# Kernel optimization log

Measured on AMD Instinct MI355X. Metric: run time of the kernel, lower is better.

The kernel has to match this reference:

```python
import jax, jax.numpy as jnp
import numpy as np

NHEAD = 8
DC = 32
IN_CHS = 2 * NHEAD  # cross_coverage and self_coverage both True
EPS = 1e-5  # BatchNorm1d default eps


def conv2d(x, w, pad):
    return jax.lax.conv_general_dilated(
        x, w, window_strides=(1, 1), padding=[(pad, pad), (pad, pad)],
        dimension_numbers=('NCHW', 'OIHW', 'NCHW'))


def setup_inputs() -> dict:
    key = jax.random.key(0)
    ks = jax.random.split(key, 10)
    b, t, H, W = 8, 256, 16, 32
    l = H * W
    prev_attn = jax.random.uniform(ks[0], (b * NHEAD, t, l), dtype=jnp.float32)
    curr_attn = jax.random.uniform(ks[1], (b * NHEAD, t, l), dtype=jnp.float32)
    key_padding_mask = jax.random.uniform(ks[2], (b, l)) < 0.25  # True = padded
    conv_w = jax.random.normal(ks[3], (DC, IN_CHS, 5, 5), jnp.float32) * 0.05
    conv_b = jnp.zeros((DC,), jnp.float32)
    proj_w = jax.random.normal(ks[4], (NHEAD, DC, 1, 1), jnp.float32) * 0.05
    g_w1 = jax.random.normal(ks[5], (IN_CHS // 2, IN_CHS, 3, 3), jnp.float32) * 0.05
    g_b1 = jnp.zeros((IN_CHS // 2,), jnp.float32)
    g_w2 = jax.random.normal(ks[6], (IN_CHS, IN_CHS // 2, 1, 1), jnp.float32) * 0.05
    g_b2 = jnp.zeros((IN_CHS,), jnp.float32)
    bn_gamma = jnp.ones((NHEAD,), jnp.float32)
    bn_beta = jnp.zeros((NHEAD,), jnp.float32)
    return dict(prev_attn=prev_attn, key_padding_mask=key_padding_mask, h=H,
                curr_attn=curr_attn, tgt_vocab=113,
                conv_w=conv_w, conv_b=conv_b, proj_w=proj_w,
                g_w1=g_w1, g_b1=g_b1, g_w2=g_w2, g_b2=g_b2,
                bn_gamma=bn_gamma, bn_beta=bn_beta)


def reference(prev_attn, key_padding_mask, h, curr_attn, tgt_vocab,
              conv_w, conv_b, proj_w, g_w1, g_b1, g_w2, g_b2, bn_gamma, bn_beta):
    n = NHEAD
    b = prev_attn.shape[0] // n
    t = curr_attn.shape[1]
    l = key_padding_mask.shape[1]
    w = l // h

    prev = prev_attn.reshape(b, n, t, l)
    curr = curr_attn.reshape(b, n, t, l)
    attns = jnp.concatenate([prev, curr], axis=1)  # [b, 2n, t, l]
    c = attns.shape[1]

    # gating network on per-step attention images: [(b t), c, h, w]
    attns_bt = attns.transpose(0, 2, 1, 3).reshape(b * t, c, h, w)
    g = jax.nn.relu(conv2d(attns_bt, g_w1, 1) + g_b1[None, :, None, None])
    g = g.mean(axis=(2, 3))  # AdaptiveAvgPool2d((1,1)) -> [(b t), c//2]
    g = jax.nn.sigmoid(jnp.einsum('bi,oi->bo', g, g_w2[:, :, 0, 0]) + g_b2)
    gate = g.reshape(b, t, c).transpose(0, 2, 1)[..., None]  # [b, c, t, 1]

    gated = attns * gate
    cum = jnp.cumsum(gated, axis=2) - gated  # exclusive cumulative coverage
    cum2d = cum.transpose(0, 2, 1, 3).reshape(b * t, c, h, w)

    mask = jnp.broadcast_to(key_padding_mask.reshape(b, 1, 1, h, w),
                            (b, t, 1, h, w)).reshape(b * t, 1, h, w)

    cov = jax.nn.relu(conv2d(cum2d, conv_w, 2) + conv_b[None, :, None, None])
    cov = jnp.where(mask, 0.0, cov)
    cov = jnp.einsum('bdhw,nd->bnhw', cov, proj_w[:, :, 0, 0])  # 1x1 proj, no bias

    # MaskBatchNorm2d: BN statistics over non-masked positions only
    nm = (~mask).astype(cov.dtype)  # [(b t), 1, h, w]
    cnt = nm.sum()
    mean = (cov * nm).sum(axis=(0, 2, 3), keepdims=True) / cnt  # per-channel
    var = (jnp.square(cov - mean) * nm).sum(axis=(0, 2, 3), keepdims=True) / cnt
    xn = (cov - mean) * jax.lax.rsqrt(var + EPS) * bn_gamma[None, :, None, None] \
        + bn_beta[None, :, None, None]
    cov = jnp.where(mask, cov, xn)  # masked positions keep pre-BN values (zeros)

    out = cov.reshape(b, t, n, l).transpose(0, 2, 1, 3).reshape(b * n, t, l)
    return out
```

## Files before the change

### kernel.cpp

```cpp
#include <hip/hip_runtime.h>
#include <hip/hip_bf16.h>

#define BB   8
#define TT   256
#define NH   8
#define CC   16
#define HH   16
#define WW   32
#define LL   512
#define DCH  32
#define GC   8

#define PSC  1928
#define PSG  1736

typedef __attribute__((ext_vector_type(8))) short s8b;
typedef __attribute__((ext_vector_type(4))) float f32x4;

__device__ __forceinline__ ushort f2bfu(float v) {
  __hip_bfloat16 h = __float2bfloat16(v);
  ushort s;
  __builtin_memcpy(&s, &h, 2);
  return s;
}

__global__ __launch_bounds__(256) void k_gen(const float* __restrict__ cw,
                                             const float* __restrict__ pw,
                                             const float* __restrict__ gw1,
                                             ushort* __restrict__ bfrag,
                                             ushort* __restrict__ pwf,
                                             ushort* __restrict__ bfragG,
                                             float* __restrict__ sums) {
  int idx = blockIdx.x * 256 + threadIdx.x;
  if (idx < 17) sums[idx] = 0.f;
  if (idx < 13312) {
    int j = idx & 7, lane = (idx >> 3) & 63, nt = (idx >> 9) & 1, s = idx >> 10;
    int quad = lane >> 4, col = lane & 15;
    int k = s * 32 + quad * 8 + j;
    int n = nt * 16 + col;
    float v = (k < 400) ? cw[(n * CC + (k & 15)) * 25 + (k >> 4)] : 0.f;
    bfrag[idx] = f2bfu(v);
  } else if (idx < 13824) {
    int i2 = idx - 13312;
    int j = i2 & 7, lane = i2 >> 3;
    int quad = lane >> 4, col = lane & 15;
    float v = (col < NH) ? pw[col * DCH + quad * 8 + j] : 0.f;
    pwf[i2] = f2bfu(v);
  } else if (idx < 16384) {
    int i3 = idx - 13824;
    int j = i3 & 7, lane = (i3 >> 3) & 63, s = i3 >> 9;
    int quad = lane >> 4, col = lane & 15;
    int k = s * 32 + quad * 8 + j;
    float v = 0.f;
    if (k < 144 && col < GC) v = gw1[(col * CC + (k & 15)) * 9 + (k >> 4)];
    bfragG[i3] = f2bfu(v);
  }
}

__global__ __launch_bounds__(256) void k_gate(
    const float* __restrict__ prev, const float* __restrict__ curr,
    const ushort* __restrict__ bfragG, const float* __restrict__ gb1,
    const float* __restrict__ gw2, const float* __restrict__ gb2,
    float* __restrict__ gate2) {
  __shared__ __align__(16) ushort img[8 * PSG];
  __shared__ float redg[64];
  __shared__ float pooled[16];

  int tid = threadIdx.x;
  int lane = tid & 63, w = tid >> 6;
  int bt = blockIdx.x;
  int b = bt >> 8, t = bt & 255;
  int quad = lane >> 4, col = lane & 15;
  int qh = quad >> 1, icb = (quad & 1) * 8;

  for (int i = tid; i < PSG; i += 256) ((uint4*)img)[i] = (uint4){0, 0, 0, 0};
  __syncthreads();

#pragma unroll
  for (int it = 0; it < 4; ++it) {
#pragma unroll
    for (int e = 0; e < 2; ++e) {
      int W = ((it * 4 + w) * 2 + e) * 64 + lane;
      int cp = W >> 8, pp = W & 255;
      int l0 = pp * 2;
      const float* src = (cp < 4) ? prev : curr;
      int chb = (cp & 3) * 2;
      const float* p0 = src + ((size_t)(b * NH + chb) * TT + t) * LL + l0;
      float2 fa = *(const float2*)p0;
      float2 fb = *(const float2*)(p0 + TT * LL);
      unsigned lo = (unsigned)f2bfu(fa.x) | ((unsigned)f2bfu(fb.x) << 16);
      unsigned hi = (unsigned)f2bfu(fa.y) | ((unsigned)f2bfu(fb.y) << 16);
      int r = l0 >> 5, x = l0 & 31;
      int slot = (r + 1) * 48 + 8 + x;
      *(uint2*)&img[cp * PSG + slot * 2] = (uint2){lo, hi};
    }
  }
  __syncthreads();

  f32x4 acc[8];
#pragma unroll
  for (int mi = 0; mi < 8; ++mi) acc[mi] = (f32x4){0.f, 0.f, 0.f, 0.f};
  int mtbase = w * 8;
  int ab[8];
#pragma unroll
  for (int mi = 0; mi < 8; ++mi) {
    int mt = mtbase + mi;
    int py = mt >> 1, px = ((mt & 1) << 4) + col;
    ab[mi] = (icb >> 1) * PSG + (py * 48 + 7 + px) * 2;
  }
  const int offE[5] = {0, 2, 49, 96, 98};
  const int offO[5] = {1, 48, 50, 97, 98};
  const s8b* bG = (const s8b*)bfragG;
#pragma unroll
  for (int s = 0; s < 5; ++s) {
    s8b bf = bG[s * 64 + lane];
    int off2 = (qh ? offO[s] : offE[s]) * 2;
#pragma unroll
    for (int mi = 0; mi < 8; ++mi) {
      union { unsigned u[4]; s8b v; } A;
      int a0 = ab[mi] + off2;
#pragma unroll
      for (int p = 0; p < 4; ++p) A.u[p] = *(const unsigned*)&img[a0 + p * PSG];
      acc[mi] = __builtin_amdgcn_mfma_f32_16x16x32_bf16(A.v, bf, acc[mi], 0, 0, 0);
    }
  }

  float gb1c = (col < GC) ? gb1[col] : 0.f;
  float s = 0.f;
#pragma unroll
  for (int mi = 0; mi < 8; ++mi)
#pragma unroll
    for (int r = 0; r < 4; ++r) s += fmaxf(acc[mi][r] + gb1c, 0.f);
  s += __shfl_down(s, 16, 64);
  s += __shfl_down(s, 32, 64);
  if (lane < 16) redg[w * 16 + lane] = s;
  __syncthreads();
  if (tid < 16)
    pooled[tid] = (redg[tid] + redg[16 + tid] + redg[32 + tid] + redg[48 + tid]) *
                  (1.0f / (float)LL);
  __syncthreads();
  if (tid < 16) {
    float z = gb2[tid];
#pragma unroll
    for (int i = 0; i < GC; ++i) z = fmaf(pooled[i], gw2[tid * GC + i], z);
    gate2[(b * CC + tid) * TT + t] = 1.f / (1.f + __expf(-z));
  }
}

__global__ __launch_bounds__(256) void k_cumA(const float* __restrict__ prev,
                                              const float* __restrict__ curr,
                                              const float* __restrict__ gate2,
                                              float* __restrict__ csum) {
  int idx = blockIdx.x * 256 + threadIdx.x;
  int l = idx & 511, tc = (idx >> 9) & 7, c = (idx >> 12) & 15, b = idx >> 16;
  const float* src = (c < NH) ? prev : curr;
  const float* a = src + ((size_t)(b * NH + (c & 7)) * TT + tc * 32) * LL + l;
  const float* g = gate2 + (b * CC + c) * TT + tc * 32;
  float s = 0.f;
#pragma unroll 8
  for (int j = 0; j < 32; ++j) s = fmaf(a[(size_t)j * LL], g[j], s);
  csum[((b * CC + c) * 8 + tc) * LL + l] = s;
}

__global__ __launch_bounds__(256) void k_cumB(const float* __restrict__ prev,
                                              const float* __restrict__ curr,
                                              const float* __restrict__ gate2,
                                              const float* __restrict__ csum,
                                              ushort* __restrict__ cum) {
  int idx = blockIdx.x * 256 + threadIdx.x;
  int l = idx & 511, tc = (idx >> 9) & 7, c = (idx >> 12) & 15, b = idx >> 16;
  float run = 0.f;
  const float* cs = csum + ((b * CC + c) * 8) * LL + l;
  for (int u = 0; u < tc; ++u) run += cs[u * LL];
  const float* src = (c < NH) ? prev : curr;
  const float* a = src + ((size_t)(b * NH + (c & 7)) * TT + tc * 32) * LL + l;
  const float* g = gate2 + (b * CC + c) * TT + tc * 32;
  ushort* o = cum + ((size_t)(b * CC + c) * TT + tc * 32) * LL + l;
#pragma unroll 4
  for (int j = 0; j < 32; ++j) {
    o[(size_t)j * LL] = f2bfu(run);
    run = fmaf(a[(size_t)j * LL], g[j], run);
  }
}

__global__ __launch_bounds__(256, 2) void k_cov(
    const ushort* __restrict__ cum, const ushort* __restrict__ bfrag,
    const ushort* __restrict__ pwf, const float* __restrict__ cb,
    const int* __restrict__ mask, float* __restrict__ out,
    float* __restrict__ sums) {
  __shared__ __align__(16) ushort img[8 * PSC];
  __shared__ __align__(16) ushort scr[4 * 640];
  __shared__ float redp[128];
  __shared__ float redc[4];

  int tid = threadIdx.x;
  int lane = tid & 63, w = tid >> 6;
  int bt = blockIdx.x;
  int b = bt >> 8, t = bt & 255;
  int quad = lane >> 4, col = lane & 15;
  int qh = quad >> 1, icb = (quad & 1) * 8;

  for (int i = tid; i < PSC; i += 256) ((uint4*)img)[i] = (uint4){0, 0, 0, 0};
  __syncthreads();

#pragma unroll
  for (int it = 0; it < 4; ++it) {
#pragma unroll
    for (int e = 0; e < 2; ++e) {
      int W = ((it * 4 + w) * 2 + e) * 64 + lane;
      int cp = W >> 8, pp = W & 255;
      int l0 = pp * 2;
      const ushort* p0 = cum + ((size_t)(b * CC + cp * 2) * TT + t) * LL + l0;
      unsigned a = *(const unsigned*)p0;
      unsigned bb2 = *(const unsigned*)(p0 + TT * LL);
      unsigned lo = (a & 0xFFFFu) | (bb2 << 16);
      unsigned hi = (a >> 16) | (bb2 & 0xFFFF0000u);
      int r = l0 >> 5, x = l0 & 31;
      int slot = (r + 2) * 48 + 8 + x;
      *(uint2*)&img[cp * PSC + slot * 2] = (uint2){lo, hi};
    }
  }
  __syncthreads();

  f32x4 acc[8][2];
#pragma unroll
  for (int mi = 0; mi < 8; ++mi) {
    acc[mi][0] = (f32x4){0.f, 0.f, 0.f, 0.f};
    acc[mi][1] = (f32x4){0.f, 0.f, 0.f, 0.f};
  }
  int mtbase = w * 8;
  int ab[8];
#pragma unroll
  for (int mi = 0; mi < 8; ++mi) {
    int mt = mtbase + mi;
    int py = mt >> 1, px = ((mt & 1) << 4) + col;
    ab[mi] = (icb >> 1) * PSC + (py * 48 + 6 + px) * 2;
  }
  const int offE[13] = {0, 2, 4, 49, 51, 96, 98, 100, 145, 147, 192, 194, 196};
  const int offO[13] = {1, 3, 48, 50, 52, 97, 99, 144, 146, 148, 193, 195, 196};
  const s8b* bfr = (const s8b*)bfrag;
#pragma unroll
  for (int s = 0; s < 13; ++s) {
    s8b bf0 = bfr[(s * 2) * 64 + lane];
    s8b bf1 = bfr[(s * 2 + 1) * 64 + lane];
    int off2 = (qh ? offO[s] : offE[s]) * 2;
#pragma unroll
    for (int mi = 0; mi < 8; ++mi) {
      union { unsigned u[4]; s8b v; } A;
      int a0 = ab[mi] + off2;
#pragma unroll
      for (int p = 0; p < 4; ++p) A.u[p] = *(const unsigned*)&img[a0 + p * PSC];
      acc[mi][0] = __builtin_amdgcn_mfma_f32_16x16x32_bf16(A.v, bf0, acc[mi][0], 0, 0, 0);
      acc[mi][1] = __builtin_amdgcn_mfma_f32_16x16x32_bf16(A.v, bf1, acc[mi][1], 0, 0, 0);
    }
  }

  int wb = w * 640;
  float cb0 = cb[col], cb1 = cb[col + 16];
  s8b pf = ((const s8b*)pwf)[lane];
  float psum = 0.f, psq = 0.f, pcnt = 0.f;
  float* outbase = out + ((size_t)(b * NH + col) * TT + t) * LL;
  const int* mrow = mask + b * LL;
#pragma unroll
  for (int mi = 0; mi < 8; ++mi) {
    int mt = mtbase + mi;
    ushort w0[4], w1[4];
#pragma unroll
    for (int r = 0; r < 4; ++r) {
      w0[r] = f2bfu(fmaxf(acc[mi][0][r] + cb0, 0.f));
      w1[r] = f2bfu(fmaxf(acc[mi][1][r] + cb1, 0.f));
    }
    uint2 pk0, pk1;
    __builtin_memcpy(&pk0, w0, 8);
    __builtin_memcpy(&pk1, w1, 8);
    *(uint2*)&scr[wb + col * 20 + quad * 4] = pk0;
    *(uint2*)&scr[wb + (col + 16) * 20 + quad * 4] = pk1;
    ushort u[8];
#pragma unroll
    for (int e = 0; e < 8; ++e) u[e] = scr[wb + (quad * 8 + e) * 20 + col];
    s8b a2;
    __builtin_memcpy(&a2, u, 16);
    f32x4 zero = {0.f, 0.f, 0.f, 0.f};
    f32x4 d2 = __builtin_amdgcn_mfma_f32_16x16x32_bf16(a2, pf, zero, 0, 0, 0);
    int4 m4 = *(const int4*)(mrow + mt * 16 + quad * 4);
    float k0 = m4.x ? 0.f : 1.f;
    float k1 = m4.y ? 0.f : 1.f;
    float k2 = m4.z ? 0.f : 1.f;
    float k3 = m4.w ? 0.f : 1.f;
    if (col < NH) {
      float* op = outbase + mt * 16 + quad * 4;
      float v0 = d2[0] * k0; op[0] = v0; psum += v0; psq += v0 * v0;
      float v1 = d2[1] * k1; op[1] = v1; psum += v1; psq += v1 * v1;
      float v2 = d2[2] * k2; op[2] = v2; psum += v2; psq += v2 * v2;
      float v3 = d2[3] * k3; op[3] = v3; psum += v3; psq += v3 * v3;
    }
    if (col == 0) pcnt += k0 + k1 + k2 + k3;
  }

  psum += __shfl_down(psum, 16, 64); psum += __shfl_down(psum, 32, 64);
  psq  += __shfl_down(psq, 16, 64);  psq  += __shfl_down(psq, 32, 64);
  pcnt += __shfl_down(pcnt, 16, 64); pcnt += __shfl_down(pcnt, 32, 64);
  if (lane < 16) {
    redp[(w * 16 + lane) * 2] = psum;
    redp[(w * 16 + lane) * 2 + 1] = psq;
    if (lane == 0) redc[w] = pcnt;
  }
  __syncthreads();
  if (tid < 17) {
    float v;
    if (tid < 8) {
      v = redp[tid * 2] + redp[(16 + tid) * 2] + redp[(32 + tid) * 2] + redp[(48 + tid) * 2];
    } else if (tid < 16) {
      int nh = tid - 8;
      v = redp[nh * 2 + 1] + redp[(16 + nh) * 2 + 1] + redp[(32 + nh) * 2 + 1] + redp[(48 + nh) * 2 + 1];
    } else {
      v = redc[0] + redc[1] + redc[2] + redc[3];
    }
    atomicAdd(&sums[tid], v);
  }
}

__global__ __launch_bounds__(256) void k_bn(
    float* __restrict__ out, const float* __restrict__ sums,
    const int* __restrict__ mask, const float* __restrict__ gamma,
    const float* __restrict__ beta) {
  __shared__ float sc[NH], sh[NH];
  int tid = threadIdx.x;
  if (tid < NH) {
    float cnt = sums[16];
    float mean = sums[tid] / cnt;
    float var = sums[NH + tid] / cnt - mean * mean;
    float inv = rsqrtf(var + 1e-5f) * gamma[tid];
    sc[tid] = inv;
    sh[tid] = fmaf(-mean, inv, beta[tid]);
  }
  __syncthreads();
  size_t e = ((size_t)blockIdx.x * 256 + tid) * 4;
  int l = (int)(e & (LL - 1));
  int bn = (int)(e >> 17);
  int n = bn & 7, b = bn >> 3;
  const int4 mv = *(const int4*)(mask + b * LL + l);
  float4 v = *(float4*)(out + e);
  float s = sc[n], h = sh[n];
  v.x = mv.x ? v.x : fmaf(v.x, s, h);
  v.y = mv.y ? v.y : fmaf(v.y, s, h);
  v.z = mv.z ? v.z : fmaf(v.z, s, h);
  v.w = mv.w ? v.w : fmaf(v.w, s, h);
  *(float4*)(out + e) = v;
}

extern "C" void kernel_launch(void* const* d_in, const int* in_sizes, int n_in,
                              void* d_out, int out_size, void* d_ws, size_t ws_size,
                              hipStream_t stream) {
  const float* prev   = (const float*)d_in[0];
  const int*   mask   = (const int*)d_in[1];
  const float* curr   = (const float*)d_in[3];
  const float* conv_w = (const float*)d_in[5];
  const float* conv_b = (const float*)d_in[6];
  const float* proj_w = (const float*)d_in[7];
  const float* g_w1   = (const float*)d_in[8];
  const float* g_b1   = (const float*)d_in[9];
  const float* g_w2   = (const float*)d_in[10];
  const float* g_b2   = (const float*)d_in[11];
  const float* bn_g   = (const float*)d_in[12];
  const float* bn_b   = (const float*)d_in[13];
  float* out = (float*)d_out;

  char* ws = (char*)d_ws;
  ushort* bfrag  = (ushort*)(ws);
  ushort* pwf    = (ushort*)(ws + 26624);
  ushort* bfragG = (ushort*)(ws + 27648);
  float*  sums   = (float*)(ws + 32768);
  float*  gate2  = (float*)(ws + 36864);
  ushort* cum    = (ushort*)(ws + 36864 + 131072);
  float*  csum   = (float*)(ws + 36864 + 131072 + 33554432);

  k_gen<<<64, 256, 0, stream>>>(conv_w, proj_w, g_w1, bfrag, pwf, bfragG, sums);
  k_gate<<<BB * TT, 256, 0, stream>>>(prev, curr, bfragG, g_b1, g_w2, g_b2, gate2);
  k_cumA<<<2048, 256, 0, stream>>>(prev, curr, gate2, csum);
  k_cumB<<<2048, 256, 0, stream>>>(prev, curr, gate2, csum, cum);
  k_cov<<<BB * TT, 256, 0, stream>>>(cum, bfrag, pwf, conv_b, mask, out, sums);
  k_bn<<<(BB * NH * TT * LL) / (256 * 4), 256, 0, stream>>>(out, sums, mask, bn_g, bn_b);
}
```

Before: 216.7 us.

## Interleave four channels per element in cum buffer and LDS images

The intermediate cumulative-coverage buffer moves from a channel-planar bf16 layout to one that packs four channels per spatial element (b,t,channel-quad,l,4). k_cumB now computes four channels per thread and writes 8-byte packed stores, and k_cov reads those with 16-byte loads straight into LDS without repacking. LDS images in k_gate and k_cov use the same 4-channel interleave, so each MFMA A fragment comes from two 8-byte LDS reads instead of four 4-byte reads, and the launch bounds rise to 4 blocks per SM. The cost is fewer threads in k_cumB (512 blocks) and more register pressure under the tighter launch bounds.

New measurement: 225.9 us. +4.2%, slower.

```diff
diff --git a/kernel.cpp b/kernel.cpp
--- a/kernel.cpp
+++ b/kernel.cpp
@@ -11,8 +11,8 @@
 #define DCH  32
 #define GC   8
 
-#define PSC  1928
-#define PSG  1736
+#define PSC4 964
+#define PSG4 868
 
 typedef __attribute__((ext_vector_type(8))) short s8b;
 typedef __attribute__((ext_vector_type(4))) float f32x4;
@@ -57,12 +57,12 @@
   }
 }
 
-__global__ __launch_bounds__(256) void k_gate(
+__global__ __launch_bounds__(256, 4) void k_gate(
     const float* __restrict__ prev, const float* __restrict__ curr,
     const ushort* __restrict__ bfragG, const float* __restrict__ gb1,
     const float* __restrict__ gw2, const float* __restrict__ gb2,
     float* __restrict__ gate2) {
-  __shared__ __align__(16) ushort img[8 * PSG];
+  __shared__ __align__(16) ushort img[4 * PSG4 * 4];
   __shared__ float redg[64];
   __shared__ float pooled[16];
 
@@ -71,29 +71,30 @@
   int bt = blockIdx.x;
   int b = bt >> 8, t = bt & 255;
   int quad = lane >> 4, col = lane & 15;
-  int qh = quad >> 1, icb = (quad & 1) * 8;
-
-  for (int i = tid; i < PSG; i += 256) ((uint4*)img)[i] = (uint4){0, 0, 0, 0};
+  int qh = quad >> 1;
+  int p0pl = (quad & 1) * 2;
+
+  for (int i = tid; i < 1736; i += 256) ((uint4*)img)[i] = (uint4){0, 0, 0, 0};
   __syncthreads();
 
 #pragma unroll
   for (int it = 0; it < 4; ++it) {
-#pragma unroll
-    for (int e = 0; e < 2; ++e) {
-      int W = ((it * 4 + w) * 2 + e) * 64 + lane;
-      int cp = W >> 8, pp = W & 255;
-      int l0 = pp * 2;
-      const float* src = (cp < 4) ? prev : curr;
-      int chb = (cp & 3) * 2;
-      const float* p0 = src + ((size_t)(b * NH + chb) * TT + t) * LL + l0;
-      float2 fa = *(const float2*)p0;
-      float2 fb = *(const float2*)(p0 + TT * LL);
-      unsigned lo = (unsigned)f2bfu(fa.x) | ((unsigned)f2bfu(fb.x) << 16);
-      unsigned hi = (unsigned)f2bfu(fa.y) | ((unsigned)f2bfu(fb.y) << 16);
-      int r = l0 >> 5, x = l0 & 31;
-      int slot = (r + 1) * 48 + 8 + x;
-      *(uint2*)&img[cp * PSG + slot * 2] = (uint2){lo, hi};
-    }
+    int E = it * 256 + tid;
+    int cq = E >> 8, e2 = E & 255, l0 = e2 * 2;
+    const float* srcb = (cq < 2) ? prev : curr;
+    int ch0 = (cq & 1) * 4;
+    const float* p0 = srcb + ((size_t)(b * NH + ch0) * TT + t) * LL + l0;
+    float2 f0 = *(const float2*)p0;
+    float2 f1 = *(const float2*)(p0 + (size_t)TT * LL);
+    float2 f2 = *(const float2*)(p0 + (size_t)2 * TT * LL);
+    float2 f3 = *(const float2*)(p0 + (size_t)3 * TT * LL);
+    unsigned w0 = (unsigned)f2bfu(f0.x) | ((unsigned)f2bfu(f1.x) << 16);
+    unsigned w1 = (unsigned)f2bfu(f2.x) | ((unsigned)f2bfu(f3.x) << 16);
+    unsigned w2 = (unsigned)f2bfu(f0.y) | ((unsigned)f2bfu(f1.y) << 16);
+    unsigned w3 = (unsigned)f2bfu(f2.y) | ((unsigned)f2bfu(f3.y) << 16);
+    int r = l0 >> 5, x = l0 & 31;
+    int slot = (r + 1) * 48 + 8 + x;
+    *(uint4*)&img[(cq * PSG4 + slot) * 4] = (uint4){w0, w1, w2, w3};
   }
   __syncthreads();
 
@@ -106,7 +107,7 @@
   for (int mi = 0; mi < 8; ++mi) {
     int mt = mtbase + mi;
     int py = mt >> 1, px = ((mt & 1) << 4) + col;
-    ab[mi] = (icb >> 1) * PSG + (py * 48 + 7 + px) * 2;
+    ab[mi] = p0pl * PSG4 + py * 48 + 7 + px;
   }
   const int offE[5] = {0, 2, 49, 96, 98};
   const int offO[5] = {1, 48, 50, 97, 98};
@@ -114,13 +115,13 @@
 #pragma unroll
   for (int s = 0; s < 5; ++s) {
     s8b bf = bG[s * 64 + lane];
-    int off2 = (qh ? offO[s] : offE[s]) * 2;
+    int off = qh ? offO[s] : offE[s];
 #pragma unroll
     for (int mi = 0; mi < 8; ++mi) {
-      union { unsigned u[4]; s8b v; } A;
-      int a0 = ab[mi] + off2;
-#pragma unroll
-      for (int p = 0; p < 4; ++p) A.u[p] = *(const unsigned*)&img[a0 + p * PSG];
+      union { uint2 u2[2]; s8b v; } A;
+      int e0 = ab[mi] + off;
+      A.u2[0] = *(const uint2*)&img[e0 * 4];
+      A.u2[1] = *(const uint2*)&img[(e0 + PSG4) * 4];
       acc[mi] = __builtin_amdgcn_mfma_f32_16x16x32_bf16(A.v, bf, acc[mi], 0, 0, 0);
     }
   }
@@ -166,29 +167,40 @@
                                               const float* __restrict__ curr,
                                               const float* __restrict__ gate2,
                                               const float* __restrict__ csum,
-                                              ushort* __restrict__ cum) {
+                                              uint2* __restrict__ cum4) {
   int idx = blockIdx.x * 256 + threadIdx.x;
-  int l = idx & 511, tc = (idx >> 9) & 7, c = (idx >> 12) & 15, b = idx >> 16;
-  float run = 0.f;
-  const float* cs = csum + ((b * CC + c) * 8) * LL + l;
-  for (int u = 0; u < tc; ++u) run += cs[u * LL];
-  const float* src = (c < NH) ? prev : curr;
-  const float* a = src + ((size_t)(b * NH + (c & 7)) * TT + tc * 32) * LL + l;
-  const float* g = gate2 + (b * CC + c) * TT + tc * 32;
-  ushort* o = cum + ((size_t)(b * CC + c) * TT + tc * 32) * LL + l;
-#pragma unroll 4
+  int l = idx & 511, tc = (idx >> 9) & 7, cq = (idx >> 12) & 3, b = idx >> 14;
+  int c0 = cq * 4;
+  float run[4];
+  const float* cs = csum + ((size_t)(b * CC + c0) * 8) * LL + l;
+#pragma unroll
+  for (int k = 0; k < 4; ++k) {
+    float r = 0.f;
+    for (int u = 0; u < tc; ++u) r += cs[(size_t)(k * 8 + u) * LL];
+    run[k] = r;
+  }
+  const float* srcb = (cq < 2) ? prev : curr;
+  const float* a = srcb + ((size_t)(b * NH + (cq & 1) * 4) * TT + tc * 32) * LL + l;
+  const float* g = gate2 + (b * CC + c0) * TT + tc * 32;
+  uint2* o = cum4 + (((size_t)(b * TT + tc * 32) * 4 + cq) * LL + l);
+#pragma unroll 2
   for (int j = 0; j < 32; ++j) {
-    o[(size_t)j * LL] = f2bfu(run);
-    run = fmaf(a[(size_t)j * LL], g[j], run);
-  }
-}
-
-__global__ __launch_bounds__(256, 2) void k_cov(
-    const ushort* __restrict__ cum, const ushort* __restrict__ bfrag,
+    uint2 pk;
+    pk.x = (unsigned)f2bfu(run[0]) | ((unsigned)f2bfu(run[1]) << 16);
+    pk.y = (unsigned)f2bfu(run[2]) | ((unsigned)f2bfu(run[3]) << 16);
+    o[(size_t)j * 4 * LL] = pk;
+#pragma unroll
+    for (int k = 0; k < 4; ++k)
+      run[k] = fmaf(a[(size_t)(k * TT + j) * LL], g[k * TT + j], run[k]);
+  }
+}
+
+__global__ __launch_bounds__(256, 4) void k_cov(
+    const ushort* __restrict__ cum4, const ushort* __restrict__ bfrag,
     const ushort* __restrict__ pwf, const float* __restrict__ cb,
     const int* __restrict__ mask, float* __restrict__ out,
     float* __restrict__ sums) {
-  __shared__ __align__(16) ushort img[8 * PSC];
+  __shared__ __align__(16) ushort img[4 * PSC4 * 4];
   __shared__ __align__(16) ushort scr[4 * 640];
   __shared__ float redp[128];
   __shared__ float redc[4];
@@ -198,27 +210,21 @@
   int bt = blockIdx.x;
   int b = bt >> 8, t = bt & 255;
   int quad = lane >> 4, col = lane & 15;
-  int qh = quad >> 1, icb = (quad & 1) * 8;
-
-  for (int i = tid; i < PSC; i += 256) ((uint4*)img)[i] = (uint4){0, 0, 0, 0};
-  __syncthreads();
-
+  int qh = quad >> 1;
+  int p0pl = (quad & 1) * 2;
+
+  for (int i = tid; i < 1928; i += 256) ((uint4*)img)[i] = (uint4){0, 0, 0, 0};
+  __syncthreads();
+
+  const ushort* cbase = cum4 + (size_t)(b * TT + t) * 4 * LL * 4;
 #pragma unroll
   for (int it = 0; it < 4; ++it) {
-#pragma unroll
-    for (int e = 0; e < 2; ++e) {
-      int W = ((it * 4 + w) * 2 + e) * 64 + lane;
-      int cp = W >> 8, pp = W & 255;
-      int l0 = pp * 2;
-      const ushort* p0 = cum + ((size_t)(b * CC + cp * 2) * TT + t) * LL + l0;
-      unsigned a = *(const unsigned*)p0;
-      unsigned bb2 = *(const unsigned*)(p0 + TT * LL);
-      unsigned lo = (a & 0xFFFFu) | (bb2 << 16);
-      unsigned hi = (a >> 16) | (bb2 & 0xFFFF0000u);
-      int r = l0 >> 5, x = l0 & 31;
-      int slot = (r + 2) * 48 + 8 + x;
-      *(uint2*)&img[cp * PSC + slot * 2] = (uint2){lo, hi};
-    }
+    int E = it * 256 + tid;
+    int cq = E >> 8, e2 = E & 255, l0 = e2 * 2;
+    uint4 v = *(const uint4*)(cbase + (cq * LL + l0) * 4);
+    int r = l0 >> 5, x = l0 & 31;
+    int slot = (r + 2) * 48 + 8 + x;
+    *(uint4*)&img[(cq * PSC4 + slot) * 4] = v;
   }
   __syncthreads();
 
@@ -234,7 +240,7 @@
   for (int mi = 0; mi < 8; ++mi) {
     int mt = mtbase + mi;
     int py = mt >> 1, px = ((mt & 1) << 4) + col;
-    ab[mi] = (icb >> 1) * PSC + (py * 48 + 6 + px) * 2;
+    ab[mi] = p0pl * PSC4 + py * 48 + 6 + px;
   }
   const int offE[13] = {0, 2, 4, 49, 51, 96, 98, 100, 145, 147, 192, 194, 196};
   const int offO[13] = {1, 3, 48, 50, 52, 97, 99, 144, 146, 148, 193, 195, 196};
@@ -243,13 +249,13 @@
   for (int s = 0; s < 13; ++s) {
     s8b bf0 = bfr[(s * 2) * 64 + lane];
     s8b bf1 = bfr[(s * 2 + 1) * 64 + lane];
-    int off2 = (qh ? offO[s] : offE[s]) * 2;
+    int off = qh ? offO[s] : offE[s];
 #pragma unroll
     for (int mi = 0; mi < 8; ++mi) {
-      union { unsigned u[4]; s8b v; } A;
-      int a0 = ab[mi] + off2;
-#pragma unroll
-      for (int p = 0; p < 4; ++p) A.u[p] = *(const unsigned*)&img[a0 + p * PSC];
+      union { uint2 u2[2]; s8b v; } A;
+      int e0 = ab[mi] + off;
+      A.u2[0] = *(const uint2*)&img[e0 * 4];
+      A.u2[1] = *(const uint2*)&img[(e0 + PSC4) * 4];
       acc[mi][0] = __builtin_amdgcn_mfma_f32_16x16x32_bf16(A.v, bf0, acc[mi][0], 0, 0, 0);
       acc[mi][1] = __builtin_amdgcn_mfma_f32_16x16x32_bf16(A.v, bf1, acc[mi][1], 0, 0, 0);
     }
@@ -372,13 +378,14 @@
   ushort* bfragG = (ushort*)(ws + 27648);
   float*  sums   = (float*)(ws + 32768);
   float*  gate2  = (float*)(ws + 36864);
-  ushort* cum    = (ushort*)(ws + 36864 + 131072);
+  uint2*  cum4   = (uint2*)(ws + 36864 + 131072);
   float*  csum   = (float*)(ws + 36864 + 131072 + 33554432);
 
   k_gen<<<64, 256, 0, stream>>>(conv_w, proj_w, g_w1, bfrag, pwf, bfragG, sums);
   k_gate<<<BB * TT, 256, 0, stream>>>(prev, curr, bfragG, g_b1, g_w2, g_b2, gate2);
   k_cumA<<<2048, 256, 0, stream>>>(prev, curr, gate2, csum);
-  k_cumB<<<2048, 256, 0, stream>>>(prev, curr, gate2, csum, cum);
-  k_cov<<<BB * TT, 256, 0, stream>>>(cum, bfrag, pwf, conv_b, mask, out, sums);
+  k_cumB<<<512, 256, 0, stream>>>(prev, curr, gate2, csum, cum4);
+  k_cov<<<BB * TT, 256, 0, stream>>>((const ushort*)cum4, bfrag, pwf, conv_b,
+                                     mask, out, sums);
   k_bn<<<(BB * NH * TT * LL) / (256 * 4), 256, 0, stream>>>(out, sums, mask, bn_g, bn_b);
 }
```
